# Kernel optimization log

Measured on AMD Instinct MI355X. Metric: run time of the kernel, lower is better.

The kernel has to match this reference:

```python
import jax, jax.numpy as jnp
import numpy as np

VOCAB = 5000; EMB = 300; AUDIO = 74; HID = 128
D1 = 16; D2 = 16; DIM = D1 * D2
UNITS = 128; CELL = 64; OUT = 1
B = 32; S = 32
NGRAMS = (1, 3)


def _lstm(x, w_ih, w_hh, b_ih, b_hh):
    # PyTorch LSTMCell semantics, gate order i, f, g, o
    Bb = x.shape[0]; H = w_hh.shape[1]
    def step(carry, xt):
        h, c = carry
        gates = xt @ w_ih.T + h @ w_hh.T + b_ih + b_hh
        i, f, g, o = jnp.split(gates, 4, axis=-1)
        c = jax.nn.sigmoid(f) * c + jax.nn.sigmoid(i) * jnp.tanh(g)
        h = jax.nn.sigmoid(o) * jnp.tanh(c)
        return (h, c), h
    init = (jnp.zeros((Bb, H), x.dtype), jnp.zeros((Bb, H), x.dtype))
    _, hs = jax.lax.scan(step, init, jnp.swapaxes(x, 0, 1))
    return jnp.swapaxes(hs, 0, 1)  # (B, S, H)


def _windows(x, n):
    # zero-padded n-gram windows: (B, S, d) -> (B, S, n, d)
    xp = jnp.pad(x, ((0, 0), (0, n - 1), (0, 0)))
    s = x.shape[1]
    return jnp.stack([xp[:, k:k + s, :] for k in range(n)], axis=2)


def setup_inputs() -> dict:
    key = jax.random.key(0)
    ks = jax.random.split(key, 26)
    g = lambda i, shape, sc=0.05: jax.random.normal(ks[i], shape, dtype=jnp.float32) * sc
    return dict(
        word_indexes=jax.random.randint(ks[0], (B, S), 0, VOCAB),
        audio=jax.random.normal(ks[1], (B, S, AUDIO), dtype=jnp.float32),
        lookup_table=g(2, (VOCAB, EMB), 0.5),
        phase_tab0=g(3, (VOCAB, D1), 3.14),
        phase_tab1=g(4, (VOCAB, D2), 3.14),
        w_ih=g(5, (4 * HID, EMB)), w_hh=g(6, (4 * HID, HID)),
        b_ih=g(7, (4 * HID,)), b_hh=g(8, (4 * HID,)),
        w_lin=g(9, (D1, HID)), b_lin=g(10, (D1,)),
        w1=g(11, (D2, AUDIO)), b1=g(12, (D2,)),
        w2=g(13, (D2, D2)), b2=g(14, (D2,)),
        w3=g(15, (D2, D2)), b3=g(16, (D2,)),
        modality_weights=jnp.zeros((2,), jnp.float32),
        meas_r=g(17, (UNITS, DIM), 0.5), meas_i=g(18, (UNITS, DIM), 0.5),
        fw1=g(19, (CELL, UNITS)), fb1=g(20, (CELL,)),
        fw2=g(21, (CELL, CELL)), fb2=g(22, (CELL,)),
        fw3=g(23, (OUT, CELL)), fb3=jnp.zeros((OUT,), jnp.float32),
    )


def reference(word_indexes, audio, lookup_table, phase_tab0, phase_tab1,
              w_ih, w_hh, b_ih, b_hh, w_lin, b_lin,
              w1, b1, w2, b2, w3, b3,
              modality_weights, meas_r, meas_i,
              fw1, fb1, fw2, fb2, fw3, fb3):
    eps = 1e-10
    # amplitude subnets (dropout rates are 0 / eval mode)
    text = lookup_table[word_indexes]                      # (B,S,EMB)
    h = _lstm(text, w_ih, w_hh, b_ih, b_hh)
    amp0 = h @ w_lin.T + b_lin                             # (B,S,D1)
    a = jax.nn.relu(audio @ w1.T + b1)
    a = jax.nn.relu(a @ w2.T + b2)
    amp1 = jax.nn.relu(a @ w3.T + b3)                      # (B,S,D2)
    ph0 = phase_tab0[word_indexes]
    ph1 = phase_tab1[word_indexes]

    def branch(amp, ph):
        norm = jnp.linalg.norm(amp, axis=-1, keepdims=True)
        ampn = amp / (norm + eps)
        return norm, ampn * jnp.cos(ph), ampn * jnp.sin(ph)

    n0, r0, i0 = branch(amp0, ph0)
    n1, r1, i1 = branch(amp1, ph1)
    mw = jax.nn.softmax(modality_weights)
    weight = mw[0] * n0 + mw[1] * n1                       # (B,S,1)

    # sequential complex tensor product across modalities,
    # starting from (real=1, imag=1) as in the original code
    tpr = r0 - i0
    tpi = r0 + i0
    real = jnp.einsum('bsi,bsj->bsij', tpr, r1) - jnp.einsum('bsi,bsj->bsij', tpi, i1)
    imag = jnp.einsum('bsi,bsj->bsij', tpr, i1) + jnp.einsum('bsi,bsj->bsij', tpi, r1)
    real = real.reshape(B, S, DIM)
    imag = imag.reshape(B, S, DIM)

    # measurement kernel: unit-norm complex vectors
    kn = jnp.sqrt(jnp.sum(meas_r ** 2 + meas_i ** 2, axis=-1, keepdims=True)) + eps
    vr = meas_r / kn
    vi = meas_i / kn

    probs = []
    for n in NGRAMS:
        wr = _windows(real, n)                             # (B,S,n,DIM)
        wi = _windows(imag, n)
        ww = jax.nn.softmax(_windows(weight, n)[..., 0], axis=-1)  # (B,S,n)
        # complex mixture: rho = sum_n w_n |v_n><v_n|
        rho_r = (jnp.einsum('bsn,bsni,bsnj->bsij', ww, wr, wr)
                 + jnp.einsum('bsn,bsni,bsnj->bsij', ww, wi, wi))
        rho_i = (jnp.einsum('bsn,bsni,bsnj->bsij', ww, wi, wr)
                 - jnp.einsum('bsn,bsni,bsnj->bsij', ww, wr, wi))
        # measurement: Re(v^H rho v) per unit
        m = (jnp.einsum('bsij,ui,uj->bsu', rho_r, vr, vr)
             + jnp.einsum('bsij,ui,uj->bsu', rho_r, vi, vi)
             + jnp.einsum('bsij,ui,uj->bsu', rho_i, vi, vr)
             - jnp.einsum('bsij,ui,uj->bsu', rho_i, vr, vi))
        probs.append(m)
    probs = jnp.concatenate(probs, axis=1)                 # (B, S*len(NGRAMS), UNITS)
    feat = jnp.max(probs, axis=1)                          # 'max' pooling
    y = jax.nn.relu(feat @ fw1.T + fb1)
    y = jax.nn.relu(y @ fw2.T + fb2)
    return y @ fw3.T + fb3                                 # (B, OUT)
```

## Files before the change

kernel.cpp:

```cpp
#include <hip/hip_runtime.h>
#include <math.h>


static constexpr unsigned XW0_OFF  = 0u;
static constexpr unsigned XW1_OFF  = 524288u;
static constexpr unsigned HOUT_OFF = 1048576u;
static constexpr unsigned XMAT_OFF = HOUT_OFF + 131072u;
static constexpr unsigned WT_OFF   = XMAT_OFF + 524288u;
static constexpr unsigned VPP_OFF  = WT_OFF + 1024u;
static constexpr unsigned PP_OFF   = VPP_OFF + 131072u;
static constexpr unsigned PP_HALF  = 262144u;

__global__ __launch_bounds__(256) void k1_xw_gemm(
    const int* __restrict__ widx, const float* __restrict__ lut,
    const float* __restrict__ w_ih, const float* __restrict__ b_ih,
    const float* __restrict__ b_hh,
    const float* __restrict__ mr, const float* __restrict__ mi,
    float* __restrict__ ws)
{
  const int bid = blockIdx.x;
  const int t = threadIdx.x;

  if (bid >= 256) {
    const int u = bid - 256;
    float r  = mr[u * 256 + t];
    float ii = mi[u * 256 + t];
    float sq = r * r + ii * ii;
    #pragma unroll
    for (int off = 1; off < 64; off <<= 1) sq += __shfl_xor(sq, off);
    __shared__ float wsum[4];
    if ((t & 63) == 0) wsum[t >> 6] = sq;
    __syncthreads();
    float tot = wsum[0] + wsum[1] + wsum[2] + wsum[3];
    float inv = 1.0f / (sqrtf(tot) + 1e-10f);
    float vr = r * inv, vi = ii * inv;
    float* vpp = ws + VPP_OFF;
    vpp[(2 * u) * 512 + t]           = vr;
    vpp[(2 * u) * 512 + 256 + t]     = vi;
    vpp[(2 * u + 1) * 512 + t]       = -vi;
    vpp[(2 * u + 1) * 512 + 256 + t] = vr;
    return;
  }

  const int rb = bid & 15, cb = (bid >> 4) & 7, kq = bid >> 7;
  const int R = rb * 64, C = cb * 64;
  const int kbase_g = kq * 152;
  const int ktot = kq ? 148 : 152;

  __shared__ alignas(16) float As[32][68];
  __shared__ alignas(16) float Ws[32][68];

  float acc[4][4] = {};
  const int r0 = (t & 15) * 4, j0 = (t >> 4) * 4;

  for (int kt = 0; kt < 5; ++kt) {
    int kl = ktot - kt * 32; if (kl > 32) kl = 32;
    #pragma unroll
    for (int pass = 0; pass < 2; ++pass) {
      int rr = (t >> 3) + pass * 32;
      int kk4 = (t & 7) * 4;
      float4 av = make_float4(0.f, 0.f, 0.f, 0.f);
      float4 wv = make_float4(0.f, 0.f, 0.f, 0.f);
      if (kk4 < kl) {
        int gk = kbase_g + kt * 32 + kk4;
        int word = widx[R + rr];
        av = *(const float4*)&lut[word * 300 + gk];
        wv = *(const float4*)&w_ih[(C + rr) * 300 + gk];
      }
      As[kk4 + 0][rr] = av.x; As[kk4 + 1][rr] = av.y;
      As[kk4 + 2][rr] = av.z; As[kk4 + 3][rr] = av.w;
      Ws[kk4 + 0][rr] = wv.x; Ws[kk4 + 1][rr] = wv.y;
      Ws[kk4 + 2][rr] = wv.z; Ws[kk4 + 3][rr] = wv.w;
    }
    __syncthreads();
    #pragma unroll
    for (int k = 0; k < 32; ++k) {
      float4 a4 = *(const float4*)&As[k][r0];
      float4 w4 = *(const float4*)&Ws[k][j0];
      float ar[4] = {a4.x, a4.y, a4.z, a4.w};
      float wr[4] = {w4.x, w4.y, w4.z, w4.w};
      #pragma unroll
      for (int i2 = 0; i2 < 4; ++i2)
        #pragma unroll
        for (int j2 = 0; j2 < 4; ++j2)
          acc[i2][j2] = fmaf(ar[i2], wr[j2], acc[i2][j2]);
    }
    __syncthreads();
  }

  float* xw = ws + (kq ? XW1_OFF : XW0_OFF);
  #pragma unroll
  for (int i2 = 0; i2 < 4; ++i2) {
    int row = R + r0 + i2, col = C + j0;
    float4 v = make_float4(acc[i2][0], acc[i2][1], acc[i2][2], acc[i2][3]);
    if (kq == 0) {
      v.x += b_ih[col + 0] + b_hh[col + 0];
      v.y += b_ih[col + 1] + b_hh[col + 1];
      v.z += b_ih[col + 2] + b_hh[col + 2];
      v.w += b_ih[col + 3] + b_hh[col + 3];
    }
    *(float4*)&xw[row * 512 + col] = v;
  }
}

__global__ __launch_bounds__(1024, 4) void k2_lstm(
    const float* __restrict__ w_hh, float* __restrict__ ws)
{
  const int b = blockIdx.x;
  const int t = threadIdx.x;
  const int jj = t >> 3;
  const int ko = t & 7;
  const int gstar = ko & 3;
  const int shalf = ko >> 2;
  const int rot = (ko >> 1) & 3;

  float4 wreg[4][4];
  #pragma unroll
  for (int g = 0; g < 4; ++g) {
    const float* wp = w_hh + (g * 128 + jj) * 128 + ko * 16;
    #pragma unroll
    for (int cc = 0; cc < 4; ++cc) {
      int ci = (cc + rot) & 3;
      wreg[g][cc] = *(const float4*)&wp[ci * 4];
    }
  }

  const float* xw0 = ws + XW0_OFF;
  const float* xw1 = ws + XW1_OFF;
  float xg[16];
  {
    const int base = (b * 32 + shalf * 16) * 512 + gstar * 128 + jj;
    #pragma unroll
    for (int i = 0; i < 16; ++i)
      xg[i] = xw0[base + i * 512] + xw1[base + i * 512];
  }
  const float m0 = (gstar == 0) ? 1.f : 0.f;
  const float m1 = (gstar == 1) ? 1.f : 0.f;
  const float m2 = (gstar == 2) ? 1.f : 0.f;
  const float m3 = (gstar == 3) ? 1.f : 0.f;

  __shared__ alignas(16) float hbuf[2][128];
  if (t < 128) hbuf[0][t] = 0.f;
  float* hout = ws + HOUT_OFF;
  float c = 0.f;
  __syncthreads();

  #pragma unroll
  for (int s = 0; s < 32; ++s) {
    const float* hb = hbuf[s & 1] + ko * 16;
    float a0 = 0.f, a1 = 0.f, a2 = 0.f, a3 = 0.f;
    #pragma unroll
    for (int cc = 0; cc < 4; ++cc) {
      int ci = (cc + rot) & 3;
      float4 h4 = *(const float4*)&hb[ci * 4];
      a0 = fmaf(wreg[0][cc].x, h4.x, fmaf(wreg[0][cc].y, h4.y, fmaf(wreg[0][cc].z, h4.z, fmaf(wreg[0][cc].w, h4.w, a0))));
      a1 = fmaf(wreg[1][cc].x, h4.x, fmaf(wreg[1][cc].y, h4.y, fmaf(wreg[1][cc].z, h4.z, fmaf(wreg[1][cc].w, h4.w, a1))));
      a2 = fmaf(wreg[2][cc].x, h4.x, fmaf(wreg[2][cc].y, h4.y, fmaf(wreg[2][cc].z, h4.z, fmaf(wreg[2][cc].w, h4.w, a2))));
      a3 = fmaf(wreg[3][cc].x, h4.x, fmaf(wreg[3][cc].y, h4.y, fmaf(wreg[3][cc].z, h4.z, fmaf(wreg[3][cc].w, h4.w, a3))));
    }
    {
      float xv = ((s >> 4) == shalf) ? xg[s & 15] : 0.f;
      a0 = fmaf(xv, m0, a0);
      a1 = fmaf(xv, m1, a1);
      a2 = fmaf(xv, m2, a2);
      a3 = fmaf(xv, m3, a3);
    }
    a0 += __shfl_xor(a0, 1); a0 += __shfl_xor(a0, 2); a0 += __shfl_xor(a0, 4);
    a1 += __shfl_xor(a1, 1); a1 += __shfl_xor(a1, 2); a1 += __shfl_xor(a1, 4);
    a2 += __shfl_xor(a2, 1); a2 += __shfl_xor(a2, 2); a2 += __shfl_xor(a2, 4);
    a3 += __shfl_xor(a3, 1); a3 += __shfl_xor(a3, 2); a3 += __shfl_xor(a3, 4);
    float si = 1.f / (1.f + __expf(-a0));
    float sf = 1.f / (1.f + __expf(-a1));
    float tg = 1.f - 2.f / (1.f + __expf(2.f * a2));
    float so = 1.f / (1.f + __expf(-a3));
    c = sf * c + si * tg;
    float tc = 1.f - 2.f / (1.f + __expf(2.f * c));
    float hn = so * tc;
    if (ko == 0) {
      hbuf[(s + 1) & 1][jj] = hn;
      hout[(b * 32 + s) * 128 + jj] = hn;
    }
    __syncthreads();
  }
}

__global__ __launch_bounds__(256) void k3_mix(
    const int* __restrict__ widx, const float* __restrict__ audio,
    const float* __restrict__ ph0t, const float* __restrict__ ph1t,
    const float* __restrict__ w_lin, const float* __restrict__ b_lin,
    const float* __restrict__ w1, const float* __restrict__ b1,
    const float* __restrict__ w2, const float* __restrict__ b2,
    const float* __restrict__ w3, const float* __restrict__ b3,
    const float* __restrict__ modw, float* __restrict__ ws)
{
  const int bs = blockIdx.x;
  const int t = threadIdx.x;
  __shared__ float amp0[16], a1s[16], a2s[16], amp1[16];
  __shared__ float tpr[16], tpi[16], r1s[16], i1s[16];
  __shared__ float nn[2];

  const float* hrow = ws + HOUT_OFF + bs * 128;
  if (t < 16) {
    float acc = b_lin[t];
    for (int u = 0; u < 128; ++u) acc = fmaf(hrow[u], w_lin[t * 128 + u], acc);
    amp0[t] = acc;
  } else if (t >= 64 && t < 80) {
    int d = t - 64;
    float acc = b1[d];
    for (int k = 0; k < 74; ++k) acc = fmaf(audio[bs * 74 + k], w1[d * 74 + k], acc);
    a1s[d] = fmaxf(acc, 0.f);
  }
  __syncthreads();
  if (t < 16) {
    float acc = b2[t];
    #pragma unroll
    for (int k = 0; k < 16; ++k) acc = fmaf(a1s[k], w2[t * 16 + k], acc);
    a2s[t] = fmaxf(acc, 0.f);
  }
  __syncthreads();
  if (t < 16) {
    float acc = b3[t];
    #pragma unroll
    for (int k = 0; k < 16; ++k) acc = fmaf(a2s[k], w3[t * 16 + k], acc);
    amp1[t] = fmaxf(acc, 0.f);
  }
  __syncthreads();
  if (t == 0) {
    float sq = 0.f;
    #pragma unroll
    for (int d = 0; d < 16; ++d) sq += amp0[d] * amp0[d];
    nn[0] = sqrtf(sq);
  } else if (t == 64) {
    float sq = 0.f;
    #pragma unroll
    for (int d = 0; d < 16; ++d) sq += amp1[d] * amp1[d];
    nn[1] = sqrtf(sq);
  }
  __syncthreads();
  const int word = widx[bs];
  if (t < 16) {
    float k0 = amp0[t] / (nn[0] + 1e-10f);
    float ph = ph0t[word * 16 + t];
    float cc = cosf(ph), ssn = sinf(ph);
    tpr[t] = k0 * (cc - ssn);
    tpi[t] = k0 * (cc + ssn);
  } else if (t >= 64 && t < 80) {
    int d = t - 64;
    float k1 = amp1[d] / (nn[1] + 1e-10f);
    float ph = ph1t[word * 16 + d];
    r1s[d] = k1 * cosf(ph);
    i1s[d] = k1 * sinf(ph);
  } else if (t == 128) {
    float e0 = __expf(modw[0]), e1 = __expf(modw[1]);
    float mw0 = e0 / (e0 + e1);
    ws[WT_OFF + bs] = mw0 * nn[0] + (1.f - mw0) * nn[1];
  }
  __syncthreads();
  const int i2 = t >> 4, j2 = t & 15;
  float rr = tpr[i2] * r1s[j2] - tpi[i2] * i1s[j2];
  float im = tpr[i2] * i1s[j2] + tpi[i2] * r1s[j2];
  float* X = ws + XMAT_OFF;
  X[bs * 512 + t] = rr;
  X[bs * 512 + 256 + t] = im;
}

__global__ __launch_bounds__(256) void k4_meas(float* __restrict__ ws)
{
  const int bid = blockIdx.x, t = threadIdx.x;
  const int rb = bid & 15, cb = (bid >> 4) & 3, kq = bid >> 6;
  const int R = rb * 64, C = cb * 64;
  const float* X = ws + XMAT_OFF;
  const float* V = ws + VPP_OFF;
  __shared__ alignas(16) float Xs[32][68];
  __shared__ alignas(16) float Vs[32][68];
  float acc[4][4] = {};
  const int r0 = (t & 15) * 4, j0 = (t >> 4) * 4;

  for (int kt = 0; kt < 4; ++kt) {
    #pragma unroll
    for (int pass = 0; pass < 2; ++pass) {
      int rr = (t >> 3) + pass * 32;
      int kk4 = (t & 7) * 4;
      int gk = kq * 128 + kt * 32 + kk4;
      float4 xv = *(const float4*)&X[(R + rr) * 512 + gk];
      float4 vv = *(const float4*)&V[(C + rr) * 512 + gk];
      Xs[kk4 + 0][rr] = xv.x; Xs[kk4 + 1][rr] = xv.y;
      Xs[kk4 + 2][rr] = xv.z; Xs[kk4 + 3][rr] = xv.w;
      Vs[kk4 + 0][rr] = vv.x; Vs[kk4 + 1][rr] = vv.y;
      Vs[kk4 + 2][rr] = vv.z; Vs[kk4 + 3][rr] = vv.w;
    }
    __syncthreads();
    #pragma unroll
    for (int k = 0; k < 32; ++k) {
      float4 a4 = *(const float4*)&Xs[k][r0];
      float4 w4 = *(const float4*)&Vs[k][j0];
      float ar[4] = {a4.x, a4.y, a4.z, a4.w};
      float wr[4] = {w4.x, w4.y, w4.z, w4.w};
      #pragma unroll
      for (int i2 = 0; i2 < 4; ++i2)
        #pragma unroll
        for (int j2 = 0; j2 < 4; ++j2)
          acc[i2][j2] = fmaf(ar[i2], wr[j2], acc[i2][j2]);
    }
    __syncthreads();
  }
  float* Pp = ws + PP_OFF + (unsigned)kq * PP_HALF;
  #pragma unroll
  for (int i2 = 0; i2 < 4; ++i2) {
    float4 v = make_float4(acc[i2][0], acc[i2][1], acc[i2][2], acc[i2][3]);
    *(float4*)&Pp[(R + r0 + i2) * 256 + C + j0] = v;
  }
}

__global__ __launch_bounds__(512) void k5_final(
    const float* __restrict__ fw1, const float* __restrict__ fb1,
    const float* __restrict__ fw2, const float* __restrict__ fb2,
    const float* __restrict__ fw3, const float* __restrict__ fb3,
    const float* __restrict__ ws, float* __restrict__ out)
{
  const int b = blockIdx.x, t = threadIdx.x;
  const int u = t & 127, sg = t >> 7;
  __shared__ float ewt[34];
  __shared__ float pl[32][128];
  __shared__ float fred[4][128];
  __shared__ float feat[128], y1[64], y2[64];
  if (t < 32) ewt[t] = __expf(ws[WT_OFF + b * 32 + t]);
  if (t >= 32 && t < 34) ewt[t] = 1.f;
  __syncthreads();

  const float* Pp = ws + PP_OFF;
  #pragma unroll
  for (int i = 0; i < 8; ++i) {
    int s = sg * 8 + i;
    int bs = b * 32 + s;
    float A = 0.f, Bv = 0.f;
    #pragma unroll
    for (int kq = 0; kq < 4; ++kq) {
      A  += Pp[kq * PP_HALF + bs * 256 + 2 * u];
      Bv += Pp[kq * PP_HALF + bs * 256 + 2 * u + 1];
    }
    pl[s][u] = A * A + Bv * Bv;
  }
  __syncthreads();

  float m = -1e30f;
  #pragma unroll
  for (int i = 0; i < 8; ++i) {
    int s = sg * 8 + i;
    float p0 = pl[s][u];
    m = fmaxf(m, p0);
    float e0 = ewt[s], e1 = ewt[s + 1], e2 = ewt[s + 2];
    float num = e0 * p0;
    if (s + 1 < 32) num += e1 * pl[s + 1][u];
    if (s + 2 < 32) num += e2 * pl[s + 2][u];
    m = fmaxf(m, num / (e0 + e1 + e2));
  }
  fred[sg][u] = m;
  __syncthreads();
  if (t < 128)
    feat[t] = fmaxf(fmaxf(fred[0][t], fred[1][t]), fmaxf(fred[2][t], fred[3][t]));
  __syncthreads();
  if (t < 64) {
    float acc = fb1[t];
    for (int k = 0; k < 128; ++k) acc = fmaf(feat[k], fw1[t * 128 + k], acc);
    y1[t] = fmaxf(acc, 0.f);
  }
  __syncthreads();
  if (t < 64) {
    float acc = fb2[t];
    #pragma unroll
    for (int k = 0; k < 64; ++k) acc = fmaf(y1[k], fw2[t * 64 + k], acc);
    y2[t] = fmaxf(acc, 0.f);
  }
  __syncthreads();
  if (t == 0) {
    float acc = fb3[0];
    #pragma unroll
    for (int k = 0; k < 64; ++k) acc = fmaf(y2[k], fw3[k], acc);
    out[b] = acc;
  }
}

extern "C" void kernel_launch(void* const* d_in, const int* in_sizes, int n_in,
                              void* d_out, int out_size, void* d_ws, size_t ws_size,
                              hipStream_t stream) {
  const int*   widx  = (const int*)d_in[0];
  const float* audio = (const float*)d_in[1];
  const float* lut   = (const float*)d_in[2];
  const float* ph0   = (const float*)d_in[3];
  const float* ph1   = (const float*)d_in[4];
  const float* w_ih  = (const float*)d_in[5];
  const float* w_hh  = (const float*)d_in[6];
  const float* b_ih  = (const float*)d_in[7];
  const float* b_hh  = (const float*)d_in[8];
  const float* w_lin = (const float*)d_in[9];
  const float* b_lin = (const float*)d_in[10];
  const float* w1    = (const float*)d_in[11];
  const float* b1    = (const float*)d_in[12];
  const float* w2    = (const float*)d_in[13];
  const float* b2    = (const float*)d_in[14];
  const float* w3    = (const float*)d_in[15];
  const float* b3    = (const float*)d_in[16];
  const float* modw  = (const float*)d_in[17];
  const float* mr    = (const float*)d_in[18];
  const float* mi    = (const float*)d_in[19];
  const float* fw1   = (const float*)d_in[20];
  const float* fb1   = (const float*)d_in[21];
  const float* fw2   = (const float*)d_in[22];
  const float* fb2   = (const float*)d_in[23];
  const float* fw3   = (const float*)d_in[24];
  const float* fb3   = (const float*)d_in[25];
  float* ws  = (float*)d_ws;
  float* out = (float*)d_out;

  k1_xw_gemm<<<dim3(384), dim3(256), 0, stream>>>(widx, lut, w_ih, b_ih, b_hh, mr, mi, ws);
  k2_lstm<<<dim3(32), dim3(1024), 0, stream>>>(w_hh, ws);
  k3_mix<<<dim3(1024), dim3(256), 0, stream>>>(widx, audio, ph0, ph1, w_lin, b_lin,
                                               w1, b1, w2, b2, w3, b3, modw, ws);
  k4_meas<<<dim3(256), dim3(256), 0, stream>>>(ws);
  k5_final<<<dim3(32), dim3(512), 0, stream>>>(fw1, fb1, fw2, fb2, fw3, fb3, ws, out);
}
```

Before: 194.1 us.

## Split LSTM into matvec producer waves and gate-update consumer waves

Restructures the recurrent LSTM kernel so 8 waves each hold a 16-column slice of w_hh for all 512 gate rows and write partial dot products to shared memory. Two further waves reduce the partials, add the precomputed input projection and apply the gate nonlinearities. This replaces the intra-wave shuffle reductions and redundant gate math across 1024 threads with a shared-memory reduction. The cost is two barriers per timestep and heavier register use per thread (128 weight floats).

New measurement: 181.9 us. 1.07x faster.

```diff
diff --git a/kernel.cpp b/kernel.cpp
--- a/kernel.cpp
+++ b/kernel.cpp
@@ -103,84 +103,93 @@
   }
 }
 
-__global__ __launch_bounds__(1024, 4) void k2_lstm(
+__global__ __launch_bounds__(640, 1) void k2_lstm(
     const float* __restrict__ w_hh, float* __restrict__ ws)
 {
   const int b = blockIdx.x;
   const int t = threadIdx.x;
-  const int jj = t >> 3;
-  const int ko = t & 7;
-  const int gstar = ko & 3;
-  const int shalf = ko >> 2;
-  const int rot = (ko >> 1) & 3;
-
-  float4 wreg[4][4];
-  #pragma unroll
-  for (int g = 0; g < 4; ++g) {
-    const float* wp = w_hh + (g * 128 + jj) * 128 + ko * 16;
-    #pragma unroll
-    for (int cc = 0; cc < 4; ++cc) {
-      int ci = (cc + rot) & 3;
-      wreg[g][cc] = *(const float4*)&wp[ci * 4];
-    }
-  }
-
+  const int wv = t >> 6;
+  const int l  = t & 63;
+
+  __shared__ alignas(16) float part[8][512];
+  __shared__ alignas(16) float hbuf[2][128];
+
+  float* hout = ws + HOUT_OFF;
   const float* xw0 = ws + XW0_OFF;
   const float* xw1 = ws + XW1_OFF;
-  float xg[16];
-  {
-    const int base = (b * 32 + shalf * 16) * 512 + gstar * 128 + jj;
-    #pragma unroll
-    for (int i = 0; i < 16; ++i)
-      xg[i] = xw0[base + i * 512] + xw1[base + i * 512];
-  }
-  const float m0 = (gstar == 0) ? 1.f : 0.f;
-  const float m1 = (gstar == 1) ? 1.f : 0.f;
-  const float m2 = (gstar == 2) ? 1.f : 0.f;
-  const float m3 = (gstar == 3) ? 1.f : 0.f;
-
-  __shared__ alignas(16) float hbuf[2][128];
+
   if (t < 128) hbuf[0][t] = 0.f;
-  float* hout = ws + HOUT_OFF;
-  float c = 0.f;
-  __syncthreads();
-
-  #pragma unroll
-  for (int s = 0; s < 32; ++s) {
-    const float* hb = hbuf[s & 1] + ko * 16;
-    float a0 = 0.f, a1 = 0.f, a2 = 0.f, a3 = 0.f;
-    #pragma unroll
-    for (int cc = 0; cc < 4; ++cc) {
-      int ci = (cc + rot) & 3;
-      float4 h4 = *(const float4*)&hb[ci * 4];
-      a0 = fmaf(wreg[0][cc].x, h4.x, fmaf(wreg[0][cc].y, h4.y, fmaf(wreg[0][cc].z, h4.z, fmaf(wreg[0][cc].w, h4.w, a0))));
-      a1 = fmaf(wreg[1][cc].x, h4.x, fmaf(wreg[1][cc].y, h4.y, fmaf(wreg[1][cc].z, h4.z, fmaf(wreg[1][cc].w, h4.w, a1))));
-      a2 = fmaf(wreg[2][cc].x, h4.x, fmaf(wreg[2][cc].y, h4.y, fmaf(wreg[2][cc].z, h4.z, fmaf(wreg[2][cc].w, h4.w, a2))));
-      a3 = fmaf(wreg[3][cc].x, h4.x, fmaf(wreg[3][cc].y, h4.y, fmaf(wreg[3][cc].z, h4.z, fmaf(wreg[3][cc].w, h4.w, a3))));
-    }
-    {
-      float xv = ((s >> 4) == shalf) ? xg[s & 15] : 0.f;
-      a0 = fmaf(xv, m0, a0);
-      a1 = fmaf(xv, m1, a1);
-      a2 = fmaf(xv, m2, a2);
-      a3 = fmaf(xv, m3, a3);
-    }
-    a0 += __shfl_xor(a0, 1); a0 += __shfl_xor(a0, 2); a0 += __shfl_xor(a0, 4);
-    a1 += __shfl_xor(a1, 1); a1 += __shfl_xor(a1, 2); a1 += __shfl_xor(a1, 4);
-    a2 += __shfl_xor(a2, 1); a2 += __shfl_xor(a2, 2); a2 += __shfl_xor(a2, 4);
-    a3 += __shfl_xor(a3, 1); a3 += __shfl_xor(a3, 2); a3 += __shfl_xor(a3, 4);
-    float si = 1.f / (1.f + __expf(-a0));
-    float sf = 1.f / (1.f + __expf(-a1));
-    float tg = 1.f - 2.f / (1.f + __expf(2.f * a2));
-    float so = 1.f / (1.f + __expf(-a3));
-    c = sf * c + si * tg;
-    float tc = 1.f - 2.f / (1.f + __expf(2.f * c));
-    float hn = so * tc;
-    if (ko == 0) {
+
+  if (wv < 8) {
+    float4 wA[4][4], wB[4][4];
+    #pragma unroll
+    for (int g = 0; g < 4; ++g) {
+      const float* pA = w_hh + (g * 128 + l) * 128 + wv * 16;
+      const float* pB = w_hh + (g * 128 + 64 + l) * 128 + wv * 16;
+      #pragma unroll
+      for (int c = 0; c < 4; ++c) {
+        wA[g][c] = *(const float4*)&pA[c * 4];
+        wB[g][c] = *(const float4*)&pB[c * 4];
+      }
+    }
+    #pragma unroll
+    for (int g = 0; g < 4; ++g)
+      #pragma unroll
+      for (int c = 0; c < 4; ++c) {
+        asm volatile("" : "+v"(wA[g][c].x), "+v"(wA[g][c].y), "+v"(wA[g][c].z), "+v"(wA[g][c].w));
+        asm volatile("" : "+v"(wB[g][c].x), "+v"(wB[g][c].y), "+v"(wB[g][c].z), "+v"(wB[g][c].w));
+      }
+    __syncthreads();
+    const float* hbase = &hbuf[0][0];
+    for (int s = 0; s < 32; ++s) {
+      const float* hb = hbase + (s & 1) * 128 + wv * 16;
+      float aA0 = 0.f, aA1 = 0.f, aA2 = 0.f, aA3 = 0.f;
+      float aB0 = 0.f, aB1 = 0.f, aB2 = 0.f, aB3 = 0.f;
+      #pragma unroll
+      for (int c = 0; c < 4; ++c) {
+        float4 h4 = *(const float4*)&hb[c * 4];
+        aA0 = fmaf(wA[0][c].x, h4.x, fmaf(wA[0][c].y, h4.y, fmaf(wA[0][c].z, h4.z, fmaf(wA[0][c].w, h4.w, aA0))));
+        aA1 = fmaf(wA[1][c].x, h4.x, fmaf(wA[1][c].y, h4.y, fmaf(wA[1][c].z, h4.z, fmaf(wA[1][c].w, h4.w, aA1))));
+        aA2 = fmaf(wA[2][c].x, h4.x, fmaf(wA[2][c].y, h4.y, fmaf(wA[2][c].z, h4.z, fmaf(wA[2][c].w, h4.w, aA2))));
+        aA3 = fmaf(wA[3][c].x, h4.x, fmaf(wA[3][c].y, h4.y, fmaf(wA[3][c].z, h4.z, fmaf(wA[3][c].w, h4.w, aA3))));
+        aB0 = fmaf(wB[0][c].x, h4.x, fmaf(wB[0][c].y, h4.y, fmaf(wB[0][c].z, h4.z, fmaf(wB[0][c].w, h4.w, aB0))));
+        aB1 = fmaf(wB[1][c].x, h4.x, fmaf(wB[1][c].y, h4.y, fmaf(wB[1][c].z, h4.z, fmaf(wB[1][c].w, h4.w, aB1))));
+        aB2 = fmaf(wB[2][c].x, h4.x, fmaf(wB[2][c].y, h4.y, fmaf(wB[2][c].z, h4.z, fmaf(wB[2][c].w, h4.w, aB2))));
+        aB3 = fmaf(wB[3][c].x, h4.x, fmaf(wB[3][c].y, h4.y, fmaf(wB[3][c].z, h4.z, fmaf(wB[3][c].w, h4.w, aB3))));
+      }
+      *(float4*)&part[wv][l * 4]       = make_float4(aA0, aA1, aA2, aA3);
+      *(float4*)&part[wv][256 + l * 4] = make_float4(aB0, aB1, aB2, aB3);
+      __syncthreads();
+      __syncthreads();
+    }
+  } else {
+    const int jj = (wv - 8) * 64 + l;
+    float c = 0.f;
+    __syncthreads();
+    for (int s = 0; s < 32; ++s) {
+      const int base = (b * 32 + s) * 512 + jj;
+      float x0 = xw0[base +   0] + xw1[base +   0];
+      float x1 = xw0[base + 128] + xw1[base + 128];
+      float x2 = xw0[base + 256] + xw1[base + 256];
+      float x3 = xw0[base + 384] + xw1[base + 384];
+      __syncthreads();
+      float g0 = x0, g1 = x1, g2 = x2, g3 = x3;
+      #pragma unroll
+      for (int w = 0; w < 8; ++w) {
+        float4 p = *(const float4*)&part[w][jj * 4];
+        g0 += p.x; g1 += p.y; g2 += p.z; g3 += p.w;
+      }
+      float si = 1.f / (1.f + __expf(-g0));
+      float sf = 1.f / (1.f + __expf(-g1));
+      float tg = 1.f - 2.f / (1.f + __expf(2.f * g2));
+      float so = 1.f / (1.f + __expf(-g3));
+      c = sf * c + si * tg;
+      float tc = 1.f - 2.f / (1.f + __expf(2.f * c));
+      float hn = so * tc;
       hbuf[(s + 1) & 1][jj] = hn;
       hout[(b * 32 + s) * 128 + jj] = hn;
-    }
-    __syncthreads();
+      __syncthreads();
+    }
   }
 }
 
@@ -414,7 +423,7 @@
   float* out = (float*)d_out;
 
   k1_xw_gemm<<<dim3(384), dim3(256), 0, stream>>>(widx, lut, w_ih, b_ih, b_hh, mr, mi, ws);
-  k2_lstm<<<dim3(32), dim3(1024), 0, stream>>>(w_hh, ws);
+  k2_lstm<<<dim3(32), dim3(640), 0, stream>>>(w_hh, ws);
   k3_mix<<<dim3(1024), dim3(256), 0, stream>>>(widx, audio, ph0, ph1, w_lin, b_lin,
                                                w1, b1, w2, b2, w3, b3, modw, ws);
   k4_meas<<<dim3(256), dim3(256), 0, stream>>>(ws);
```
